# Performance work log

Measured on AMD Instinct MI355X. Metric: run time of the kernel, lower is better.

The kernel has to match this reference:

```python
import jax, jax.numpy as jnp
import numpy as np

N_HEADS = 32
N_KV_HEADS = 8
HEAD_DIM = 128
N_QUERY = N_HEADS // N_KV_HEADS  # 4
ROPE_BASE = 10000.0


def _rope_tables(seq_len, head_dim):
    # inv freqs over pairs of channels (Llama-style interleaved complex rotation)
    inv_freq = 1.0 / (ROPE_BASE ** (jnp.arange(0, head_dim, 2, dtype=jnp.float32) / head_dim))
    t = jnp.arange(seq_len, dtype=jnp.float32)
    ang = t[:, None] * inv_freq[None, :]           # [s, d/2]
    return jnp.cos(ang)[None, :, None, :], jnp.sin(ang)[None, :, None, :]  # [1,s,1,d/2]


def _apply_rope(x, cos, sin):
    # x: [b, s, h, d]; consecutive channel pairs are (real, imag)
    xr = x[..., 0::2]
    xi = x[..., 1::2]
    out_r = xr * cos - xi * sin
    out_i = xr * sin + xi * cos
    return jnp.stack([out_r, out_i], axis=-1).reshape(x.shape)


def setup_inputs() -> dict:
    key = jax.random.key(0)
    kx, kq, kk, kv, ko = jax.random.split(key, 5)
    dim = 4096
    kv_dim = N_KV_HEADS * HEAD_DIM
    scale = 0.02
    return {
        "x": jax.random.normal(kx, (2, 2048, dim), dtype=jnp.float32),
        "wq": jax.random.normal(kq, (dim, dim), dtype=jnp.float32) * scale,
        "wk": jax.random.normal(kk, (dim, kv_dim), dtype=jnp.float32) * scale,
        "wv": jax.random.normal(kv, (dim, kv_dim), dtype=jnp.float32) * scale,
        "wo": jax.random.normal(ko, (dim, dim), dtype=jnp.float32) * scale,
    }


def reference(x, wq, wk, wv, wo):
    b, s, _ = x.shape
    xq = (x @ wq).reshape(b, s, N_HEADS, HEAD_DIM)
    xk = (x @ wk).reshape(b, s, N_KV_HEADS, HEAD_DIM)
    xv = (x @ wv).reshape(b, s, N_KV_HEADS, HEAD_DIM)

    cos, sin = _rope_tables(s, HEAD_DIM)
    xq = _apply_rope(xq, cos, sin)
    xk = _apply_rope(xk, cos, sin)

    # GQA without materializing the KV expand: group query heads per kv head.
    qh = xq.reshape(b, s, N_KV_HEADS, N_QUERY, HEAD_DIM)
    scores = jnp.einsum('bsgnd,btgd->bgnst', qh, xk) / jnp.sqrt(
        jnp.asarray(HEAD_DIM, dtype=xq.dtype))  # [b,g,n,s,t]

    # causal mask: -inf above diagonal
    causal = jnp.arange(s)[:, None] >= jnp.arange(s)[None, :]
    scores = jnp.where(causal[None, None, None, :, :], scores, -jnp.inf)

    att = jax.nn.softmax(scores.astype(jnp.float32), axis=-1).astype(xq.dtype)
    out = jnp.einsum('bgnst,btgd->bsgnd', att, xv).reshape(b, s, N_HEADS * HEAD_DIM)
    return out @ wo
```

## Files before the change

### kernel.cpp

```cpp
#include <hip/hip_runtime.h>
#include <hip/hip_bf16.h>

typedef __attribute__((ext_vector_type(8))) short short8;
typedef __attribute__((ext_vector_type(4))) float f32x4;

#define GLD16(gp, lp) __builtin_amdgcn_global_load_lds( \
    (const __attribute__((address_space(1))) unsigned int*)(gp), \
    (__attribute__((address_space(3))) unsigned int*)(lp), 16, 0, 0)

static __device__ __forceinline__ float bf2f(unsigned short u) {
    union { unsigned int i; float f; } v; v.i = ((unsigned int)u) << 16; return v.f;
}
static __device__ __forceinline__ short f2bf(float f) {
    union { float f; unsigned int i; } v; v.f = f;
    unsigned int r = v.i + 0x7FFFu + ((v.i >> 16) & 1u);
    return (short)(r >> 16);
}
static __device__ __forceinline__ unsigned int pack2bf(float lo, float hi) {
    return ((unsigned int)(unsigned short)f2bf(hi) << 16) | (unsigned int)(unsigned short)f2bf(lo);
}

__global__ void cast_f32_bf16(const float* __restrict__ src, short* __restrict__ dst, int n) {
    int i = (blockIdx.x * 256 + threadIdx.x) * 4;
    if (i >= n) return;
    float4 v = *(const float4*)(src + i);
    short4 o;
    o.x = f2bf(v.x); o.y = f2bf(v.y); o.z = f2bf(v.z); o.w = f2bf(v.w);
    *(short4*)(dst + i) = o;
}

__global__ void transpose_cast(const float* __restrict__ src, short* __restrict__ dst,
                               int N, int dstStride) {
    __shared__ float tile[32][33];
    int k0 = blockIdx.x * 32, n0 = blockIdx.y * 32;
    int t = threadIdx.x, c = t & 31, r = t >> 5;
#pragma unroll
    for (int p = 0; p < 4; ++p)
        tile[r + p * 8][c] = src[(size_t)(k0 + r + p * 8) * N + n0 + c];
    __syncthreads();
#pragma unroll
    for (int p = 0; p < 4; ++p)
        dst[(size_t)(n0 + r + p * 8) * dstStride + k0 + c] = f2bf(tile[c][r + p * 8]);
}

__global__ void transpose_v(const short* __restrict__ qkv, short* __restrict__ vt) {
    __shared__ short tile[32][33];
    int s0 = blockIdx.x * 32, d0 = blockIdx.y * 32;
    int bh = blockIdx.z;
    int b = bh >> 3, h = bh & 7;
    const short* src = qkv + (size_t)b * 2048 * 6144 + 5120 + h * 128;
    short* dst = vt + (size_t)bh * 128 * 2048;
    int t = threadIdx.x, c = t & 31, r = t >> 5;
#pragma unroll
    for (int p = 0; p < 4; ++p)
        tile[r + p * 8][c] = src[(size_t)(s0 + r + p * 8) * 6144 + d0 + c];
    __syncthreads();
#pragma unroll
    for (int p = 0; p < 4; ++p)
        dst[(size_t)(d0 + r + p * 8) * 2048 + s0 + c] = tile[c][r + p * 8];
}

__global__ void rope_tables(float* __restrict__ cs) {
    int i = blockIdx.x * 256 + threadIdx.x;
    int s = i >> 6, d2 = i & 63;
    float inv = expf(-9.210340371976184f * (float)(2 * d2) * (1.0f / 128.0f));
    float ang = (float)s * inv;
    float sn, c;
    sincosf(ang, &sn, &c);
    cs[(size_t)i * 2] = c;
    cs[(size_t)i * 2 + 1] = sn;
}

template<int NH>
__global__ void rope_apply(const short* __restrict__ qkv, const float* __restrict__ cs,
                           short* __restrict__ dst, int colOff, float scale) {
    int i = blockIdx.x * 256 + threadIdx.x;
    int d2 = i & 63;
    int t2 = i >> 6;
    int h = t2 % NH;
    int bs = t2 / NH;
    int s = bs & 2047;
    int b = bs >> 11;
    unsigned int pr = *(const unsigned int*)(qkv + (size_t)bs * 6144 + colOff + h * 128 + 2 * d2);
    float xr = bf2f((unsigned short)(pr & 0xFFFFu));
    float xi = bf2f((unsigned short)(pr >> 16));
    const float* cp = cs + ((size_t)s * 64 + d2) * 2;
    float c = cp[0], sn = cp[1];
    float outr = (xr * c - xi * sn) * scale;
    float outi = (xr * sn + xi * c) * scale;
    *(unsigned int*)(dst + ((size_t)(b * NH + h) * 2048 + s) * 128 + 2 * d2) = pack2bf(outr, outi);
}

template<bool BF16OUT>
__global__ __launch_bounds__(256, 2) void gemm_bt(const short* __restrict__ A,
                                                  const short* __restrict__ Bt,
                                                  void* __restrict__ Cv,
                                                  int N, int K) {
    __shared__ short As[128 * 64];
    __shared__ short Bs[128 * 64];
    const int tid = threadIdx.x;
    const int lane = tid & 63;
    const int wid = tid >> 6;
    const int lr = lane & 15;
    const int lq = lane >> 4;
    const int m0 = blockIdx.x * 128;
    const int n0 = blockIdx.y * 128;
    const int wr = (wid >> 1) * 64;
    const int wc = (wid & 1) * 64;
    f32x4 acc[4][4];
#pragma unroll
    for (int i = 0; i < 4; ++i)
#pragma unroll
        for (int j = 0; j < 4; ++j) acc[i][j] = f32x4{0.f, 0.f, 0.f, 0.f};

    const short* aBase = A + (size_t)m0 * K;
    const short* bBase = Bt + (size_t)n0 * K;

    for (int k0 = 0; k0 < K; k0 += 64) {
#pragma unroll
        for (int j = 0; j < 4; ++j) {
            int c = (wid * 4 + j) * 64 + lane;
            int row = c >> 3;
            int cb = ((c & 7) << 4) ^ ((row & 7) << 4);
            GLD16(aBase + (size_t)row * K + k0 + (cb >> 1), As + (wid * 4 + j) * 512);
            GLD16(bBase + (size_t)row * K + k0 + (cb >> 1), Bs + (wid * 4 + j) * 512);
        }
        __syncthreads();
#pragma unroll
        for (int ks = 0; ks < 2; ++ks) {
            short8 af[4], bfr[4];
#pragma unroll
            for (int mi = 0; mi < 4; ++mi) {
                int row = wr + mi * 16 + lr;
                int cb = (ks * 64 + lq * 16) ^ ((row & 7) << 4);
                af[mi] = *(const short8*)(As + row * 64 + (cb >> 1));
            }
#pragma unroll
            for (int ni = 0; ni < 4; ++ni) {
                int row = wc + ni * 16 + lr;
                int cb = (ks * 64 + lq * 16) ^ ((row & 7) << 4);
                bfr[ni] = *(const short8*)(Bs + row * 64 + (cb >> 1));
            }
#pragma unroll
            for (int mi = 0; mi < 4; ++mi)
#pragma unroll
                for (int ni = 0; ni < 4; ++ni)
                    acc[mi][ni] = __builtin_amdgcn_mfma_f32_16x16x32_bf16(af[mi], bfr[ni], acc[mi][ni], 0, 0, 0);
        }
        __syncthreads();
    }
#pragma unroll
    for (int mi = 0; mi < 4; ++mi)
#pragma unroll
        for (int ni = 0; ni < 4; ++ni)
#pragma unroll
            for (int r = 0; r < 4; ++r) {
                int row = m0 + wr + mi * 16 + lq * 4 + r;
                int col = n0 + wc + ni * 16 + lr;
                float v = acc[mi][ni][r];
                if constexpr (BF16OUT) ((short*)Cv)[(size_t)row * N + col] = f2bf(v);
                else                   ((float*)Cv)[(size_t)row * N + col] = v;
            }
}

__global__ __launch_bounds__(256, 4) void attn_kernel(const short* __restrict__ Qr,
                                                      const short* __restrict__ Kr,
                                                      const short* __restrict__ Vt,
                                                      short* __restrict__ Out) {
    __shared__ short Ks[64 * 128];
    __shared__ short Vs[128 * 64];
    __shared__ short Ps[4 * 1024];
    const int qb = 31 - blockIdx.x;
    const int bh = blockIdx.y;
    const int b = bh >> 5;
    const int qh = bh & 31;
    const int kvh = qh >> 2;
    const int tid = threadIdx.x;
    const int lane = tid & 63;
    const int wid = tid >> 6;
    const int lr = lane & 15;
    const int lq = lane >> 4;

    const short* qbase = Qr + ((size_t)bh * 2048 + qb * 64 + wid * 16) * 128;
    short8 qf[4];
#pragma unroll
    for (int ks = 0; ks < 4; ++ks)
        qf[ks] = *(const short8*)(qbase + lr * 128 + ks * 32 + lq * 8);

    const short* kbase = Kr + (size_t)(b * 8 + kvh) * 2048 * 128;
    const short* vbase = Vt + (size_t)(b * 8 + kvh) * 128 * 2048;

    float m_run = -INFINITY, l_run = 0.0f;
    f32x4 o_acc[8];
#pragma unroll
    for (int d = 0; d < 8; ++d) o_acc[d] = f32x4{0.f, 0.f, 0.f, 0.f};

    short* pw = Ps + wid * 1024;
    for (int kb = 0; kb <= qb; ++kb) {
        const int s0 = kb * 64;
#pragma unroll
        for (int j = 0; j < 4; ++j) {
            int c = (wid * 4 + j) * 64 + lane;
            int krow = c >> 4;
            int kcb = ((c & 15) << 4) ^ ((krow & 7) << 4);
            GLD16(kbase + (size_t)(s0 + krow) * 128 + (kcb >> 1), Ks + (wid * 4 + j) * 512);
            int vrow = c >> 3;
            int vcb = ((c & 7) << 4) ^ ((vrow & 7) << 4);
            GLD16(vbase + (size_t)vrow * 2048 + s0 + (vcb >> 1), Vs + (wid * 4 + j) * 512);
        }
        __syncthreads();

        f32x4 st[4];
#pragma unroll
        for (int ct = 0; ct < 4; ++ct) st[ct] = f32x4{0.f, 0.f, 0.f, 0.f};
#pragma unroll
        for (int ct = 0; ct < 4; ++ct) {
#pragma unroll
            for (int ks = 0; ks < 4; ++ks) {
                int row = ct * 16 + lr;
                int cb = (ks * 64 + lq * 16) ^ ((row & 7) << 4);
                short8 kf = *(const short8*)(Ks + row * 128 + (cb >> 1));
                st[ct] = __builtin_amdgcn_mfma_f32_16x16x32_bf16(kf, qf[ks], st[ct], 0, 0, 0);
            }
        }

        if (kb == qb) {
#pragma unroll
            for (int ct = 0; ct < 4; ++ct)
#pragma unroll
                for (int r = 0; r < 4; ++r)
                    if (ct * 16 + lq * 4 + r > wid * 16 + lr) st[ct][r] = -INFINITY;
        }

        float mx = fmaxf(fmaxf(fmaxf(st[0][0], st[0][1]), fmaxf(st[0][2], st[0][3])),
                         fmaxf(fmaxf(st[1][0], st[1][1]), fmaxf(st[1][2], st[1][3])));
        mx = fmaxf(mx, fmaxf(fmaxf(fmaxf(st[2][0], st[2][1]), fmaxf(st[2][2], st[2][3])),
                             fmaxf(fmaxf(st[3][0], st[3][1]), fmaxf(st[3][2], st[3][3]))));
        mx = fmaxf(mx, __shfl_xor(mx, 16, 64));
        mx = fmaxf(mx, __shfl_xor(mx, 32, 64));

        const bool defer = __all(mx - m_run <= 8.0f);
        float mN, alpha;
        if (defer) { mN = m_run; alpha = 1.0f; }
        else       { mN = fmaxf(m_run, mx); alpha = __expf(m_run - mN); }

        float p[4][4];
        float rsum = 0.0f;
#pragma unroll
        for (int ct = 0; ct < 4; ++ct)
#pragma unroll
            for (int r = 0; r < 4; ++r) {
                p[ct][r] = __expf(st[ct][r] - mN);
                rsum += p[ct][r];
            }
        rsum += __shfl_xor(rsum, 16, 64);
        rsum += __shfl_xor(rsum, 32, 64);
        l_run = l_run * alpha + rsum;
        m_run = mN;

#pragma unroll
        for (int ct = 0; ct < 4; ++ct) {
            uint2 w;
            w.x = pack2bf(p[ct][0], p[ct][1]);
            w.y = pack2bf(p[ct][2], p[ct][3]);
            int off = (ct * 32 + lq * 8) ^ ((lr & 7) << 4);
            *(uint2*)(pw + ((lr * 128 + off) >> 1)) = w;
        }

        if (!defer) {
            float av[4];
#pragma unroll
            for (int r = 0; r < 4; ++r) av[r] = __shfl(alpha, lq * 4 + r, 64);
#pragma unroll
            for (int dt = 0; dt < 8; ++dt)
#pragma unroll
                for (int r = 0; r < 4; ++r) o_acc[dt][r] *= av[r];
        }

        short8 pa[2];
#pragma unroll
        for (int kk = 0; kk < 2; ++kk)
            pa[kk] = *(const short8*)(pw + ((lr * 128 + ((kk * 64 + lq * 16) ^ ((lr & 7) << 4))) >> 1));
#pragma unroll
        for (int dt = 0; dt < 8; ++dt) {
#pragma unroll
            for (int kk = 0; kk < 2; ++kk) {
                int row = dt * 16 + lr;
                int cb = (kk * 64 + lq * 16) ^ ((row & 7) << 4);
                short8 vf = *(const short8*)(Vs + row * 64 + (cb >> 1));
                o_acc[dt] = __builtin_amdgcn_mfma_f32_16x16x32_bf16(pa[kk], vf, o_acc[dt], 0, 0, 0);
            }
        }
        __syncthreads();
    }

    float lrow[4];
#pragma unroll
    for (int r = 0; r < 4; ++r) lrow[r] = __shfl(l_run, lq * 4 + r, 64);
    const size_t orow0 = (size_t)b * 2048 + qb * 64 + wid * 16;
#pragma unroll
    for (int r = 0; r < 4; ++r) {
        float inv = 1.0f / lrow[r];
#pragma unroll
        for (int dt = 0; dt < 8; ++dt) {
            size_t row = orow0 + lq * 4 + r;
            Out[row * 4096 + qh * 128 + dt * 16 + lr] = f2bf(o_acc[dt][r] * inv);
        }
    }
}


extern "C" void kernel_launch(void* const* d_in, const int* in_sizes, int n_in,
                              void* d_out, int out_size, void* d_ws, size_t ws_size,
                              hipStream_t stream) {
    const float* x  = (const float*)d_in[0];
    const float* wq = (const float*)d_in[1];
    const float* wk = (const float*)d_in[2];
    const float* wv = (const float*)d_in[3];
    const float* wo = (const float*)d_in[4];
    float* out = (float*)d_out;
    char* ws = (char*)d_ws;

    short* wt_qkv = (short*)(ws + 0);
    short* xb     = (short*)(ws + 50331648);
    short* qkv    = (short*)(ws + 83886080);
    short* wt_o   = (short*)(ws + 83886080);
    short* qr     = (short*)(ws + 134217728);
    short* kr     = (short*)(ws + 167772160);
    short* vt     = (short*)(ws + 176160768);
    float* tab    = (float*)(ws + 184549376);

    cast_f32_bf16<<<16384, 256, 0, stream>>>(x, xb, 16777216);
    transpose_cast<<<dim3(128, 128), 256, 0, stream>>>(wq, wt_qkv, 4096, 4096);
    transpose_cast<<<dim3(128, 32),  256, 0, stream>>>(wk, wt_qkv + (size_t)4096 * 4096, 1024, 4096);
    transpose_cast<<<dim3(128, 32),  256, 0, stream>>>(wv, wt_qkv + (size_t)5120 * 4096, 1024, 4096);
    rope_tables<<<512, 256, 0, stream>>>(tab);
    gemm_bt<true><<<dim3(32, 48), 256, 0, stream>>>(xb, wt_qkv, (void*)qkv, 6144, 4096);
    rope_apply<32><<<32768, 256, 0, stream>>>(qkv, tab, qr, 0, 0.08838834764831845f);
    rope_apply<8><<<8192, 256, 0, stream>>>(qkv, tab, kr, 4096, 1.0f);
    transpose_v<<<dim3(64, 4, 16), 256, 0, stream>>>(qkv, vt);
    transpose_cast<<<dim3(128, 128), 256, 0, stream>>>(wo, wt_o, 4096, 4096);
    attn_kernel<<<dim3(32, 64), 256, 0, stream>>>(qr, kr, vt, xb);
    gemm_bt<false><<<dim3(32, 32), 256, 0, stream>>>(xb, wt_o, (void*)out, 4096, 4096);
}
```

Measured before the change: 638.8 us.

## Rewrite attention with 32x32 MFMA, 128-query blocks and register-resident P

After: 597.3 us. -6.5%, faster.

```diff
diff --git a/kernel.cpp b/kernel.cpp
--- a/kernel.cpp
+++ b/kernel.cpp
@@ -3,6 +3,7 @@
 
 typedef __attribute__((ext_vector_type(8))) short short8;
 typedef __attribute__((ext_vector_type(4))) float f32x4;
+typedef __attribute__((ext_vector_type(16))) float f32x16;
 
 #define GLD16(gp, lp) __builtin_amdgcn_global_load_lds( \
     (const __attribute__((address_space(1))) unsigned int*)(gp), \
@@ -18,6 +19,11 @@
 }
 static __device__ __forceinline__ unsigned int pack2bf(float lo, float hi) {
     return ((unsigned int)(unsigned short)f2bf(hi) << 16) | (unsigned int)(unsigned short)f2bf(lo);
+}
+static __device__ __forceinline__ unsigned int cvtpk(float lo, float hi) {
+    unsigned int w;
+    asm("v_cvt_pk_bf16_f32 %0, %1, %2" : "=v"(w) : "v"(lo), "v"(hi));
+    return w;
 }
 
 __global__ void cast_f32_bf16(const float* __restrict__ src, short* __restrict__ dst, int n) {
@@ -163,148 +169,153 @@
             }
 }
 
-__global__ __launch_bounds__(256, 4) void attn_kernel(const short* __restrict__ Qr,
+__global__ __launch_bounds__(256, 2) void attn_kernel(const short* __restrict__ Qr,
                                                       const short* __restrict__ Kr,
                                                       const short* __restrict__ Vt,
                                                       short* __restrict__ Out) {
     __shared__ short Ks[64 * 128];
     __shared__ short Vs[128 * 64];
-    __shared__ short Ps[4 * 1024];
-    const int qb = 31 - blockIdx.x;
+    const int qb = 15 - blockIdx.x;
     const int bh = blockIdx.y;
     const int b = bh >> 5;
     const int qh = bh & 31;
     const int kvh = qh >> 2;
     const int tid = threadIdx.x;
     const int lane = tid & 63;
-    const int wid = tid >> 6;
-    const int lr = lane & 15;
-    const int lq = lane >> 4;
-
-    const short* qbase = Qr + ((size_t)bh * 2048 + qb * 64 + wid * 16) * 128;
-    short8 qf[4];
-#pragma unroll
-    for (int ks = 0; ks < 4; ++ks)
-        qf[ks] = *(const short8*)(qbase + lr * 128 + ks * 32 + lq * 8);
+    const int w = tid >> 6;
+    const int l31 = lane & 31;
+    const int hi = lane >> 5;
+    const int qg0 = qb * 128 + w * 32;
+
+    const short* qbase = Qr + ((size_t)bh * 2048 + qg0 + l31) * 128 + hi * 8;
+    short8 qf[8];
+#pragma unroll
+    for (int ks = 0; ks < 8; ++ks)
+        qf[ks] = *(const short8*)(qbase + ks * 16);
 
     const short* kbase = Kr + (size_t)(b * 8 + kvh) * 2048 * 128;
     const short* vbase = Vt + (size_t)(b * 8 + kvh) * 128 * 2048;
 
     float m_run = -INFINITY, l_run = 0.0f;
-    f32x4 o_acc[8];
-#pragma unroll
-    for (int d = 0; d < 8; ++d) o_acc[d] = f32x4{0.f, 0.f, 0.f, 0.f};
-
-    short* pw = Ps + wid * 1024;
-    for (int kb = 0; kb <= qb; ++kb) {
+    f32x16 oacc[4];
+#pragma unroll
+    for (int dt = 0; dt < 4; ++dt) oacc[dt] = f32x16{0,0,0,0,0,0,0,0,0,0,0,0,0,0,0,0};
+
+    const int nkb = 2 * qb + 2;
+    for (int kb = 0; kb < nkb; ++kb) {
         const int s0 = kb * 64;
 #pragma unroll
         for (int j = 0; j < 4; ++j) {
-            int c = (wid * 4 + j) * 64 + lane;
+            int c = j * 256 + tid;
             int krow = c >> 4;
-            int kcb = ((c & 15) << 4) ^ ((krow & 7) << 4);
-            GLD16(kbase + (size_t)(s0 + krow) * 128 + (kcb >> 1), Ks + (wid * 4 + j) * 512);
+            int kcol = ((c & 15) ^ (krow & 7)) * 8;
+            GLD16(kbase + (size_t)(s0 + krow) * 128 + kcol, Ks + (size_t)c * 8);
             int vrow = c >> 3;
-            int vcb = ((c & 7) << 4) ^ ((vrow & 7) << 4);
-            GLD16(vbase + (size_t)vrow * 2048 + s0 + (vcb >> 1), Vs + (wid * 4 + j) * 512);
+            int vcol = ((c & 7) ^ (vrow & 7)) * 8;
+            GLD16(vbase + (size_t)vrow * 2048 + s0 + vcol, Vs + (size_t)c * 8);
         }
         __syncthreads();
 
-        f32x4 st[4];
-#pragma unroll
-        for (int ct = 0; ct < 4; ++ct) st[ct] = f32x4{0.f, 0.f, 0.f, 0.f};
-#pragma unroll
-        for (int ct = 0; ct < 4; ++ct) {
-#pragma unroll
-            for (int ks = 0; ks < 4; ++ks) {
-                int row = ct * 16 + lr;
-                int cb = (ks * 64 + lq * 16) ^ ((row & 7) << 4);
-                short8 kf = *(const short8*)(Ks + row * 128 + (cb >> 1));
-                st[ct] = __builtin_amdgcn_mfma_f32_16x16x32_bf16(kf, qf[ks], st[ct], 0, 0, 0);
-            }
-        }
-
-        if (kb == qb) {
-#pragma unroll
-            for (int ct = 0; ct < 4; ++ct)
-#pragma unroll
-                for (int r = 0; r < 4; ++r)
-                    if (ct * 16 + lq * 4 + r > wid * 16 + lr) st[ct][r] = -INFINITY;
-        }
-
-        float mx = fmaxf(fmaxf(fmaxf(st[0][0], st[0][1]), fmaxf(st[0][2], st[0][3])),
-                         fmaxf(fmaxf(st[1][0], st[1][1]), fmaxf(st[1][2], st[1][3])));
-        mx = fmaxf(mx, fmaxf(fmaxf(fmaxf(st[2][0], st[2][1]), fmaxf(st[2][2], st[2][3])),
-                             fmaxf(fmaxf(st[3][0], st[3][1]), fmaxf(st[3][2], st[3][3]))));
-        mx = fmaxf(mx, __shfl_xor(mx, 16, 64));
-        mx = fmaxf(mx, __shfl_xor(mx, 32, 64));
-
-        const bool defer = __all(mx - m_run <= 8.0f);
-        float mN, alpha;
-        if (defer) { mN = m_run; alpha = 1.0f; }
-        else       { mN = fmaxf(m_run, mx); alpha = __expf(m_run - mN); }
-
-        float p[4][4];
-        float rsum = 0.0f;
-#pragma unroll
-        for (int ct = 0; ct < 4; ++ct)
-#pragma unroll
-            for (int r = 0; r < 4; ++r) {
-                p[ct][r] = __expf(st[ct][r] - mN);
-                rsum += p[ct][r];
-            }
-        rsum += __shfl_xor(rsum, 16, 64);
-        rsum += __shfl_xor(rsum, 32, 64);
-        l_run = l_run * alpha + rsum;
-        m_run = mN;
-
-#pragma unroll
-        for (int ct = 0; ct < 4; ++ct) {
-            uint2 w;
-            w.x = pack2bf(p[ct][0], p[ct][1]);
-            w.y = pack2bf(p[ct][2], p[ct][3]);
-            int off = (ct * 32 + lq * 8) ^ ((lr & 7) << 4);
-            *(uint2*)(pw + ((lr * 128 + off) >> 1)) = w;
-        }
-
-        if (!defer) {
-            float av[4];
-#pragma unroll
-            for (int r = 0; r < 4; ++r) av[r] = __shfl(alpha, lq * 4 + r, 64);
-#pragma unroll
-            for (int dt = 0; dt < 8; ++dt)
-#pragma unroll
-                for (int r = 0; r < 4; ++r) o_acc[dt][r] *= av[r];
-        }
-
-        short8 pa[2];
-#pragma unroll
-        for (int kk = 0; kk < 2; ++kk)
-            pa[kk] = *(const short8*)(pw + ((lr * 128 + ((kk * 64 + lq * 16) ^ ((lr & 7) << 4))) >> 1));
-#pragma unroll
-        for (int dt = 0; dt < 8; ++dt) {
-#pragma unroll
-            for (int kk = 0; kk < 2; ++kk) {
-                int row = dt * 16 + lr;
-                int cb = (kk * 64 + lq * 16) ^ ((row & 7) << 4);
-                short8 vf = *(const short8*)(Vs + row * 64 + (cb >> 1));
-                o_acc[dt] = __builtin_amdgcn_mfma_f32_16x16x32_bf16(pa[kk], vf, o_acc[dt], 0, 0, 0);
-            }
+        if (s0 <= qg0 + 31) {
+            f32x16 st0 = f32x16{0,0,0,0,0,0,0,0,0,0,0,0,0,0,0,0};
+            f32x16 st1 = f32x16{0,0,0,0,0,0,0,0,0,0,0,0,0,0,0,0};
+            __builtin_amdgcn_s_setprio(1);
+#pragma unroll
+            for (int ks = 0; ks < 8; ++ks) {
+                int row0 = l31;
+                int ch0 = ((2 * ks + hi) ^ (row0 & 7)) * 8;
+                short8 kf0 = *(const short8*)(Ks + row0 * 128 + ch0);
+                st0 = __builtin_amdgcn_mfma_f32_32x32x16_bf16(kf0, qf[ks], st0, 0, 0, 0);
+                int row1 = 32 + l31;
+                int ch1 = ((2 * ks + hi) ^ (row1 & 7)) * 8;
+                short8 kf1 = *(const short8*)(Ks + row1 * 128 + ch1);
+                st1 = __builtin_amdgcn_mfma_f32_32x32x16_bf16(kf1, qf[ks], st1, 0, 0, 0);
+            }
+            __builtin_amdgcn_s_setprio(0);
+
+            const int q = qg0 + l31;
+            if (s0 + 63 > qg0) {
+#pragma unroll
+                for (int i = 0; i < 16; ++i) {
+                    int kvr = (i & 3) + 8 * (i >> 2) + 4 * hi;
+                    if (s0 + kvr > q)      st0[i] = -INFINITY;
+                    if (s0 + 32 + kvr > q) st1[i] = -INFINITY;
+                }
+            }
+
+            float mx = -INFINITY;
+#pragma unroll
+            for (int i = 0; i < 16; ++i) mx = fmaxf(mx, fmaxf(st0[i], st1[i]));
+            mx = fmaxf(mx, __shfl_xor(mx, 32, 64));
+
+            const bool defer = __all(mx - m_run <= 8.0f);
+            float mN, alpha;
+            if (defer) { mN = m_run; alpha = 1.0f; }
+            else       { mN = fmaxf(m_run, mx); alpha = __expf(m_run - mN); }
+
+            float p0[16], p1[16];
+            float rsum = 0.0f;
+#pragma unroll
+            for (int i = 0; i < 16; ++i) {
+                p0[i] = __expf(st0[i] - mN);
+                p1[i] = __expf(st1[i] - mN);
+                rsum += p0[i] + p1[i];
+            }
+            rsum += __shfl_xor(rsum, 32, 64);
+            l_run = l_run * alpha + rsum;
+            m_run = mN;
+            if (!defer) {
+#pragma unroll
+                for (int dt = 0; dt < 4; ++dt)
+#pragma unroll
+                    for (int i = 0; i < 16; ++i) oacc[dt][i] *= alpha;
+            }
+
+            short8 pfr[4];
+#pragma unroll
+            for (int kvs = 0; kvs < 4; ++kvs) {
+                const float* pp = (kvs < 2) ? p0 : p1;
+                const int h8 = (kvs & 1) * 8;
+                unsigned int x0 = cvtpk(pp[h8 + 0], pp[h8 + 1]);
+                unsigned int x1 = cvtpk(pp[h8 + 2], pp[h8 + 3]);
+                unsigned int y0 = cvtpk(pp[h8 + 4], pp[h8 + 5]);
+                unsigned int y1 = cvtpk(pp[h8 + 6], pp[h8 + 7]);
+                asm("v_permlane32_swap_b32 %0, %1" : "+v"(x0), "+v"(y0));
+                asm("v_permlane32_swap_b32 %0, %1" : "+v"(x1), "+v"(y1));
+                union { unsigned int u[4]; short8 s; } uu;
+                uu.u[0] = x0; uu.u[1] = x1; uu.u[2] = y0; uu.u[3] = y1;
+                pfr[kvs] = uu.s;
+            }
+
+            __builtin_amdgcn_s_setprio(1);
+#pragma unroll
+            for (int dt = 0; dt < 4; ++dt) {
+                int row = dt * 32 + l31;
+#pragma unroll
+                for (int kvs = 0; kvs < 4; ++kvs) {
+                    int ch = ((2 * kvs + hi) ^ (row & 7)) * 8;
+                    short8 vf = *(const short8*)(Vs + row * 64 + ch);
+                    oacc[dt] = __builtin_amdgcn_mfma_f32_32x32x16_bf16(vf, pfr[kvs], oacc[dt], 0, 0, 0);
+                }
+            }
+            __builtin_amdgcn_s_setprio(0);
         }
         __syncthreads();
     }
 
-    float lrow[4];
-#pragma unroll
-    for (int r = 0; r < 4; ++r) lrow[r] = __shfl(l_run, lq * 4 + r, 64);
-    const size_t orow0 = (size_t)b * 2048 + qb * 64 + wid * 16;
-#pragma unroll
-    for (int r = 0; r < 4; ++r) {
-        float inv = 1.0f / lrow[r];
-#pragma unroll
-        for (int dt = 0; dt < 8; ++dt) {
-            size_t row = orow0 + lq * 4 + r;
-            Out[row * 4096 + qh * 128 + dt * 16 + lr] = f2bf(o_acc[dt][r] * inv);
+    const float inv = 1.0f / l_run;
+    const size_t row = (size_t)b * 2048 + qg0 + l31;
+    short* obase = Out + row * 4096 + qh * 128;
+#pragma unroll
+    for (int dt = 0; dt < 4; ++dt) {
+#pragma unroll
+        for (int g = 0; g < 4; ++g) {
+            short4 o4;
+            o4.x = f2bf(oacc[dt][g * 4 + 0] * inv);
+            o4.y = f2bf(oacc[dt][g * 4 + 1] * inv);
+            o4.z = f2bf(oacc[dt][g * 4 + 2] * inv);
+            o4.w = f2bf(oacc[dt][g * 4 + 3] * inv);
+            *(short4*)(obase + dt * 32 + g * 8 + hi * 4) = o4;
         }
     }
 }
@@ -340,6 +351,6 @@
     rope_apply<8><<<8192, 256, 0, stream>>>(qkv, tab, kr, 4096, 1.0f);
     transpose_v<<<dim3(64, 4, 16), 256, 0, stream>>>(qkv, vt);
     transpose_cast<<<dim3(128, 128), 256, 0, stream>>>(wo, wt_o, 4096, 4096);
-    attn_kernel<<<dim3(32, 64), 256, 0, stream>>>(qr, kr, vt, xb);
+    attn_kernel<<<dim3(16, 64), 256, 0, stream>>>(qr, kr, vt, xb);
     gemm_bt<false><<<dim3(32, 32), 256, 0, stream>>>(xb, wt_o, (void*)out, 4096, 4096);
 }
```
